# Optimization experiments

Hardware: AMD Instinct MI355X
Metric: run time of the kernel (lower is better)

## Reference

```python
import jax, jax.numpy as jnp
import numpy as np

N, M, D = 8192, 8192, 512
TINY = jnp.finfo(jnp.float32).tiny


def setup_inputs() -> dict:
    key = jax.random.key(0)
    k1, k2 = jax.random.split(key)
    x = jax.random.normal(k1, (N, D), dtype=jnp.float32)
    x2 = jax.random.normal(k2, (M, D), dtype=jnp.float32)
    # flax self.param with ones initializer (pre-softplus raw params)
    amplitude_raw = jnp.ones((1,), dtype=jnp.float32)
    length_scale_raw = jnp.ones((D,), dtype=jnp.float32)
    return {"x": x, "x2": x2, "amplitude_raw": amplitude_raw,
            "length_scale_raw": length_scale_raw}


def reference(x, x2, amplitude_raw, length_scale_raw):
    # Parameter transforms exactly as in RBFKernelProvider.apply
    amplitude = jax.nn.softplus(amplitude_raw) + TINY          # (1,)
    length_scale = jax.nn.softplus(length_scale_raw) + TINY    # (D,)

    # rbf_kernel_fun: exp(-0.5 * sum(((x - x2)/l)^2)) * amp^2
    # GEMM rewrite of the squared scaled distance (avoids (N,M,D) intermediate):
    # ||xs_i - ys_j||^2 = ||xs_i||^2 + ||ys_j||^2 - 2 xs_i . ys_j
    xs = x / length_scale                                       # (N, D)
    ys = x2 / length_scale                                      # (M, D)
    x_sq = jnp.sum(xs * xs, axis=-1)                            # (N,)
    y_sq = jnp.sum(ys * ys, axis=-1)                            # (M,)
    cross = jnp.einsum('nd,md->nm', xs, ys)                     # (N, M) GEMM
    sq_dists = jnp.maximum(x_sq[:, None] + y_sq[None, :] - 2.0 * cross, 0.0)
    kernel_matrix = jnp.exp(-0.5 * sq_dists)                    # (N, M)
    return (amplitude ** 2) * kernel_matrix
```

## Files before the change

### kernel.cpp

```cpp
#include <hip/hip_runtime.h>

#define AS1 __attribute__((address_space(1)))
#define AS3 __attribute__((address_space(3)))

typedef __attribute__((ext_vector_type(4))) float f32x4;

static constexpr int Nn = 8192;
static constexpr int Mm = 8192;
static constexpr int Dd = 512;
static constexpr float TINY = 1.17549435082228751e-38f;

__device__ __forceinline__ float softplus_f(float x) {
    return fmaxf(x, 0.0f) + log1pf(expf(-fabsf(x)));
}

__device__ __forceinline__ void g2l16(const void* g, void* l) {
    __builtin_amdgcn_global_load_lds((const AS1 unsigned int*)g,
                                     (AS3 unsigned int*)l, 16, 0, 0);
}

__global__ __launch_bounds__(256) void scale_rows(
        const float* __restrict__ x, const float* __restrict__ x2,
        const float* __restrict__ ls_raw,
        unsigned char* __restrict__ xs, unsigned char* __restrict__ ys,
        float* __restrict__ x_sq, float* __restrict__ y_sq) {
    int wave = threadIdx.x >> 6, lane = threadIdx.x & 63;
    int row = blockIdx.x * 4 + wave;

    const float* src; unsigned char* dst; float* nrm; int r;
    if (row < Nn) {
        src = x  + (size_t)row * Dd; dst = xs + (size_t)row * 512;
        nrm = x_sq + row; r = row;
    } else {
        int m = row - Nn;
        src = x2 + (size_t)m * Dd;   dst = ys + (size_t)m * 512;
        nrm = y_sq + m; r = m;
    }

    float4 v0 = ((const float4*)src)[lane * 2];
    float4 v1 = ((const float4*)src)[lane * 2 + 1];
    float4 L0 = ((const float4*)ls_raw)[lane * 2];
    float4 L1 = ((const float4*)ls_raw)[lane * 2 + 1];

    float il[8] = {
        1.0f / (softplus_f(L0.x) + TINY), 1.0f / (softplus_f(L0.y) + TINY),
        1.0f / (softplus_f(L0.z) + TINY), 1.0f / (softplus_f(L0.w) + TINY),
        1.0f / (softplus_f(L1.x) + TINY), 1.0f / (softplus_f(L1.y) + TINY),
        1.0f / (softplus_f(L1.z) + TINY), 1.0f / (softplus_f(L1.w) + TINY) };
    float s[8] = { v0.x*il[0], v0.y*il[1], v0.z*il[2], v0.w*il[3],
                   v1.x*il[4], v1.y*il[5], v1.z*il[6], v1.w*il[7] };
    float sum = 0.0f;
#pragma unroll
    for (int i = 0; i < 8; ++i) sum += s[i] * s[i];

    int p0 = __builtin_amdgcn_cvt_pk_fp8_f32(s[0], s[1], 0, false);
    p0     = __builtin_amdgcn_cvt_pk_fp8_f32(s[2], s[3], p0, true);
    int p1 = __builtin_amdgcn_cvt_pk_fp8_f32(s[4], s[5], 0, false);
    p1     = __builtin_amdgcn_cvt_pk_fp8_f32(s[6], s[7], p1, true);

    int j    = lane >> 1;
    int phys = (j & ~3) | ((j & 3) ^ (r & 3));
    *(int2*)(dst + phys * 16 + (lane & 1) * 8) = make_int2(p0, p1);

#pragma unroll
    for (int off = 32; off > 0; off >>= 1) sum += __shfl_down(sum, off, 64);
    if (lane == 0) *nrm = sum;
}

__global__ __launch_bounds__(256) void gemm_rbf(
        const unsigned char* __restrict__ xs,
        const unsigned char* __restrict__ ys,
        const float* __restrict__ x_sq, const float* __restrict__ y_sq,
        const float* __restrict__ amp_raw, float* __restrict__ out) {

    __shared__ unsigned char sA[128 * 64];
    __shared__ unsigned char sB[128 * 64];

    const int tid  = threadIdx.x;
    const int wave = tid >> 6, lane = tid & 63;
    const int wy = wave >> 1, wx = wave & 1;
    const int lane15 = lane & 15, quad = lane >> 4;
    const int srow = lane >> 2, schunk = lane & 3;

    const size_t rowBase = (size_t)blockIdx.y * 128;
    const size_t colBase = (size_t)blockIdx.x * 128;

    f32x4 acc[4][4] = {};

    for (int kt = 0; kt < 8; ++kt) {
        __syncthreads();
        const size_t kOff = (size_t)kt * 64;
#pragma unroll
        for (int t = 0; t < 2; ++t) {
            int issue = wave * 2 + t;
            int rit = issue * 16 + srow;
            const unsigned char* ga =
                xs + (rowBase + rit) * 512 + kOff + schunk * 16;
            g2l16(ga, sA + issue * 1024);
            const unsigned char* gb =
                ys + (colBase + rit) * 512 + kOff + schunk * 16;
            g2l16(gb, sB + issue * 1024);
        }
        __syncthreads();

#pragma unroll
        for (int ks = 0; ks < 2; ++ks) {
            long long aF[4], bF[4];
#pragma unroll
            for (int ty = 0; ty < 4; ++ty) {
                int rr = wy * 64 + ty * 16 + lane15;
                int phys = (ks * 2 + (quad >> 1)) ^ (rr & 3);
                aF[ty] = *(const long long*)(sA + rr * 64 + phys * 16
                                             + (quad & 1) * 8);
            }
#pragma unroll
            for (int tx = 0; tx < 4; ++tx) {
                int rr = wx * 64 + tx * 16 + lane15;
                int phys = (ks * 2 + (quad >> 1)) ^ (rr & 3);
                bF[tx] = *(const long long*)(sB + rr * 64 + phys * 16
                                             + (quad & 1) * 8);
            }
#pragma unroll
            for (int ty = 0; ty < 4; ++ty)
#pragma unroll
                for (int tx = 0; tx < 4; ++tx)
                    acc[ty][tx] = __builtin_amdgcn_mfma_f32_16x16x32_fp8_fp8(
                        aF[ty], bF[tx], acc[ty][tx], 0, 0, 0);
        }
    }

    float a = softplus_f(amp_raw[0]) + TINY;
    const float amp2 = a * a;
#pragma unroll
    for (int ty = 0; ty < 4; ++ty) {
        const size_t r0 = rowBase + wy * 64 + ty * 16 + quad * 4;
        float xq[4];
#pragma unroll
        for (int i = 0; i < 4; ++i) xq[i] = x_sq[r0 + i];
#pragma unroll
        for (int tx = 0; tx < 4; ++tx) {
            const size_t gc = colBase + wx * 64 + tx * 16 + lane15;
            const float yq = y_sq[gc];
            float* o = out + r0 * (size_t)Mm + gc;
#pragma unroll
            for (int reg = 0; reg < 4; ++reg) {
                float sq = fmaxf(xq[reg] + yq - 2.0f * acc[ty][tx][reg], 0.0f);
                o[(size_t)reg * Mm] = amp2 * __expf(-0.5f * sq);
            }
        }
    }
}

__global__ __launch_bounds__(256) void rbf_fallback(
        const float* __restrict__ x, const float* __restrict__ x2,
        const float* __restrict__ amp_raw, const float* __restrict__ ls_raw,
        float* __restrict__ out) {
    __shared__ float il[Dd];
    __shared__ float sX[16 * Dd];
    __shared__ float sY[16 * Dd];
    int tid = threadIdx.x;
    for (int i = tid; i < Dd; i += 256)
        il[i] = 1.0f / (softplus_f(ls_raw[i]) + TINY);
    __syncthreads();
    int bR = blockIdx.y * 16, bC = blockIdx.x * 16;
    for (int i = tid; i < 16 * Dd; i += 256) {
        int r = i >> 9, c = i & (Dd - 1);
        sX[i] = x [(size_t)(bR + r) * Dd + c] * il[c];
        sY[i] = x2[(size_t)(bC + r) * Dd + c] * il[c];
    }
    __syncthreads();
    float a = softplus_f(amp_raw[0]) + TINY;
    float amp2 = a * a;
    int r = tid >> 4, c = tid & 15;
    float sq = 0.0f;
    for (int d = 0; d < Dd; ++d) {
        float df = sX[r * Dd + d] - sY[c * Dd + d];
        sq += df * df;
    }
    out[(size_t)(bR + r) * Mm + (bC + c)] = amp2 * __expf(-0.5f * sq);
}

extern "C" void kernel_launch(void* const* d_in, const int* in_sizes, int n_in,
                              void* d_out, int out_size, void* d_ws, size_t ws_size,
                              hipStream_t stream) {
    const float* x       = (const float*)d_in[0];
    const float* x2      = (const float*)d_in[1];
    const float* amp_raw = (const float*)d_in[2];
    const float* ls_raw  = (const float*)d_in[3];
    float* out = (float*)d_out;

    const size_t OFF_XSQ = 0;
    const size_t OFF_YSQ = OFF_XSQ + 8192 * 4;
    const size_t OFF_XS  = OFF_YSQ + 8192 * 4;
    const size_t OFF_YS  = OFF_XS + (size_t)Nn * Dd;
    const size_t NEED    = OFF_YS + (size_t)Mm * Dd;

    if (ws_size < NEED) {
        dim3 g(Mm / 16, Nn / 16);
        rbf_fallback<<<g, 256, 0, stream>>>(x, x2, amp_raw, ls_raw, out);
        return;
    }

    char* ws = (char*)d_ws;
    float* x_sq = (float*)(ws + OFF_XSQ);
    float* y_sq = (float*)(ws + OFF_YSQ);
    unsigned char* xs = (unsigned char*)(ws + OFF_XS);
    unsigned char* ys = (unsigned char*)(ws + OFF_YS);

    scale_rows<<<(Nn + Mm) / 4, 256, 0, stream>>>(x, x2, ls_raw, xs, ys, x_sq, y_sq);
    dim3 g(Mm / 128, Nn / 128);
    gemm_rbf<<<g, 256, 0, stream>>>(xs, ys, x_sq, y_sq, amp_raw, out);
}
```

Baseline: 353.8 us.

## Switch GEMM to gfx950 scaled 16x16x128 FP8 MFMA with 128-byte K tiles

Replaces the 16x16x32 FP8 MFMA with the MI355X-specific mfma_scale 16x16x128 f8f6f4 instruction using unit scales, so each instruction covers four times the K depth. The K tile grows from 64 to 128 bytes per row (4 iterations instead of 8), LDS buffers double, and the XOR swizzle in both the pre-scaling kernel and the LDS reads widens from 4 to 8 chunks. Intent is fewer MFMA issues, fewer barriers and wider LDS reads. It changes how K elements are assigned to lanes and relies on the swizzle matching between writer and reader.

```diff
diff --git a/kernel.cpp b/kernel.cpp
--- a/kernel.cpp
+++ b/kernel.cpp
@@ -4,6 +4,7 @@
 #define AS3 __attribute__((address_space(3)))
 
 typedef __attribute__((ext_vector_type(4))) float f32x4;
+typedef __attribute__((ext_vector_type(8))) int   i32x8;
 
 static constexpr int Nn = 8192;
 static constexpr int Mm = 8192;
@@ -59,7 +60,7 @@
     p1     = __builtin_amdgcn_cvt_pk_fp8_f32(s[6], s[7], p1, true);
 
     int j    = lane >> 1;
-    int phys = (j & ~3) | ((j & 3) ^ (r & 3));
+    int phys = (j & ~7) | ((j & 7) ^ (r & 7));
     *(int2*)(dst + phys * 16 + (lane & 1) * 8) = make_int2(p0, p1);
 
 #pragma unroll
@@ -73,27 +74,27 @@
         const float* __restrict__ x_sq, const float* __restrict__ y_sq,
         const float* __restrict__ amp_raw, float* __restrict__ out) {
 
-    __shared__ unsigned char sA[128 * 64];
-    __shared__ unsigned char sB[128 * 64];
+    __shared__ unsigned char sA[128 * 128];
+    __shared__ unsigned char sB[128 * 128];
 
     const int tid  = threadIdx.x;
     const int wave = tid >> 6, lane = tid & 63;
     const int wy = wave >> 1, wx = wave & 1;
     const int lane15 = lane & 15, quad = lane >> 4;
-    const int srow = lane >> 2, schunk = lane & 3;
+    const int srow = lane >> 3, schunk = lane & 7;
 
     const size_t rowBase = (size_t)blockIdx.y * 128;
     const size_t colBase = (size_t)blockIdx.x * 128;
 
     f32x4 acc[4][4] = {};
 
-    for (int kt = 0; kt < 8; ++kt) {
+    for (int kt = 0; kt < 4; ++kt) {
         __syncthreads();
-        const size_t kOff = (size_t)kt * 64;
-#pragma unroll
-        for (int t = 0; t < 2; ++t) {
-            int issue = wave * 2 + t;
-            int rit = issue * 16 + srow;
+        const size_t kOff = (size_t)kt * 128;
+#pragma unroll
+        for (int t = 0; t < 4; ++t) {
+            int issue = wave * 4 + t;
+            int rit = issue * 8 + srow;
             const unsigned char* ga =
                 xs + (rowBase + rit) * 512 + kOff + schunk * 16;
             g2l16(ga, sA + issue * 1024);
@@ -103,29 +104,34 @@
         }
         __syncthreads();
 
-#pragma unroll
-        for (int ks = 0; ks < 2; ++ks) {
-            long long aF[4], bF[4];
-#pragma unroll
-            for (int ty = 0; ty < 4; ++ty) {
-                int rr = wy * 64 + ty * 16 + lane15;
-                int phys = (ks * 2 + (quad >> 1)) ^ (rr & 3);
-                aF[ty] = *(const long long*)(sA + rr * 64 + phys * 16
-                                             + (quad & 1) * 8);
-            }
-#pragma unroll
-            for (int tx = 0; tx < 4; ++tx) {
-                int rr = wx * 64 + tx * 16 + lane15;
-                int phys = (ks * 2 + (quad >> 1)) ^ (rr & 3);
-                bF[tx] = *(const long long*)(sB + rr * 64 + phys * 16
-                                             + (quad & 1) * 8);
-            }
-#pragma unroll
-            for (int ty = 0; ty < 4; ++ty)
-#pragma unroll
-                for (int tx = 0; tx < 4; ++tx)
-                    acc[ty][tx] = __builtin_amdgcn_mfma_f32_16x16x32_fp8_fp8(
-                        aF[ty], bF[tx], acc[ty][tx], 0, 0, 0);
+        i32x8 bF[4];
+#pragma unroll
+        for (int tx = 0; tx < 4; ++tx) {
+            int rr = wx * 64 + tx * 16 + lane15;
+            int x7 = rr & 7;
+            int p0 = (quad * 2 + 0) ^ x7, p1 = (quad * 2 + 1) ^ x7;
+            int4 lo = *(const int4*)(sB + rr * 128 + p0 * 16);
+            int4 hi = *(const int4*)(sB + rr * 128 + p1 * 16);
+            i32x8 f; f[0]=lo.x; f[1]=lo.y; f[2]=lo.z; f[3]=lo.w;
+                     f[4]=hi.x; f[5]=hi.y; f[6]=hi.z; f[7]=hi.w;
+            bF[tx] = f;
+        }
+#pragma unroll
+        for (int ty = 0; ty < 4; ++ty) {
+            int rr = wy * 64 + ty * 16 + lane15;
+            int x7 = rr & 7;
+            int p0 = (quad * 2 + 0) ^ x7, p1 = (quad * 2 + 1) ^ x7;
+            int4 lo = *(const int4*)(sA + rr * 128 + p0 * 16);
+            int4 hi = *(const int4*)(sA + rr * 128 + p1 * 16);
+            i32x8 aF; aF[0]=lo.x; aF[1]=lo.y; aF[2]=lo.z; aF[3]=lo.w;
+                      aF[4]=hi.x; aF[5]=hi.y; aF[6]=hi.z; aF[7]=hi.w;
+#pragma unroll
+            for (int tx = 0; tx < 4; ++tx)
+                acc[ty][tx] = __builtin_amdgcn_mfma_scale_f32_16x16x128_f8f6f4(
+                    aF, bF[tx], acc[ty][tx],
+                    0 , 0 ,
+                    0, 0x7F7F7F7F,
+                    0, 0x7F7F7F7F);
         }
     }
 
```

After: 327.4 us. -7.4%, faster.
